# Kernel tuning notes

Measured on AMD Instinct MI355X. Metric: run time of the kernel, lower is better.

## Reference

```python
import jax, jax.numpy as jnp
import numpy as np

N = 50000      # nodes
D_IN = 128     # input_dim
D_OUT = 128    # output_dim
K = 4          # number of core adjacencies (len(adj_list))
E = 600000     # edges per adjacency
LN_EPS = 1e-5


def setup_inputs() -> dict:
    key = jax.random.key(0)
    ks = jax.random.split(key, 9)
    x = jax.random.normal(ks[0], (N, D_IN), dtype=jnp.float32)
    rows = jax.random.randint(ks[1], (K, E), 0, N, dtype=jnp.int32)
    cols = jax.random.randint(ks[2], (K, E), 0, N, dtype=jnp.int32)
    vals = jax.random.uniform(ks[3], (K, E), dtype=jnp.float32)
    std = 1.0 / np.sqrt(D_OUT)  # GRUCell.reset_parameters uniform(-std, std)
    w_x = jax.random.uniform(ks[4], (3 * D_OUT, D_IN), jnp.float32, -std, std)
    b_x = jax.random.uniform(ks[5], (3 * D_OUT,), jnp.float32, -std, std)
    w_h = jax.random.uniform(ks[6], (3 * D_OUT, D_OUT), jnp.float32, -std, std)
    b_h = jax.random.uniform(ks[7], (3 * D_OUT,), jnp.float32, -std, std)
    ln_g = jnp.ones((D_OUT,), jnp.float32)
    ln_b = jnp.zeros((D_OUT,), jnp.float32)
    return {"x": x, "vals": vals, "w_x": w_x, "b_x": b_x, "w_h": w_h,
            "b_h": b_h, "ln_g": ln_g, "ln_b": ln_b, "rows": rows, "cols": cols}


def reference(x, vals, w_x, b_x, w_h, b_h, ln_g, ln_b, rows, cols):
    n = x.shape[0]

    def step(h, inp):
        r, c, v = inp  # COO sparse adj for this diffusion step
        # torch.sparse.mm(adj, x): gather source rows, scale, scatter-add to dest
        msg = v[:, None] * x[c]                              # [E, D_IN]
        res = jax.nn.relu(jax.ops.segment_sum(msg, r, num_segments=n))
        # GRUCell
        gate_x = res @ w_x.T + b_x                           # [N, 3*D_OUT]
        gate_h = h @ w_h.T + b_h
        i_r, i_i, i_n = jnp.split(gate_x, 3, axis=1)
        h_r, h_i, h_n = jnp.split(gate_h, 3, axis=1)
        resetgate = jax.nn.sigmoid(i_r + h_r)
        inputgate = jax.nn.sigmoid(i_i + h_i)
        newgate = jnp.tanh(i_n + resetgate * h_n)
        hy = newgate + inputgate * (h - newgate)
        return hy, None

    # adj_list = adj_list[::-1]
    h0 = jnp.zeros((n, D_OUT), dtype=x.dtype)
    h, _ = jax.lax.scan(step, h0, (rows[::-1], cols[::-1], vals[::-1]))
    # LayerNorm(output_dim)
    mean = jnp.mean(h, axis=-1, keepdims=True)
    var = jnp.var(h, axis=-1, keepdims=True)
    return (h - mean) / jnp.sqrt(var + LN_EPS) * ln_g + ln_b
```

## Files before the change

kernel.cpp:

```cpp
#include <hip/hip_runtime.h>
#include <cstdint>

#define NN 50000
#define DD 128
#define EE 600000
#define NBK 49
#define BCAP 14336

typedef __attribute__((ext_vector_type(8))) short bf16x8;
typedef __attribute__((ext_vector_type(4))) float f32x4;

__device__ __forceinline__ float sigmoid_f(float x) {
    return 1.0f / (1.0f + __expf(-x));
}
__device__ __forceinline__ float tanh_f(float x) {
    float e = __expf(-2.0f * fabsf(x));
    float t = (1.0f - e) / (1.0f + e);
    return copysignf(t, x);
}
__device__ __forceinline__ unsigned short bf16_rn(float v) {
    unsigned u = __float_as_uint(v);
    u = u + 0x7fffu + ((u >> 16) & 1u);
    return (unsigned short)(u >> 16);
}
__device__ __forceinline__ float bf16_tf(unsigned short h) {
    return __uint_as_float(((unsigned)h) << 16);
}

__global__ __launch_bounds__(256) void pack_w_kernel(const float* __restrict__ wx,
                                                     const float* __restrict__ wh,
                                                     unsigned short* __restrict__ Wp) {
    int idx = blockIdx.x * 256 + threadIdx.x;
    if (idx >= 24 * 512 * 32) return;
    int k8 = idx & 31;
    int n = (idx >> 5) & 511;
    int kb = idx >> 14;
    int grp = kb >> 2;
    int k = (kb & 3) * 32 + k8;
    float v = 0.f;
    if (grp < 3) {
        if (n < 384) v = wx[n * 128 + k];
    } else {
        if (n < 256) v = wh[n * 128 + k];
        else if (n >= 384) v = wh[(n - 128) * 128 + k];
    }
    unsigned short hi = bf16_rn(v);
    bool lo = (grp == 2) || (grp == 5);
    Wp[idx] = lo ? bf16_rn(v - bf16_tf(hi)) : hi;
}


__global__ __launch_bounds__(256) void bhist_kernel(const int* __restrict__ rows,
                                                    int* __restrict__ bcnt4) {
    __shared__ int lc[NBK];
    const int tid = threadIdx.x;
    const int k = blockIdx.y;
    const int e0 = blockIdx.x * 2048;
    if (tid < NBK) lc[tid] = 0;
    __syncthreads();
    #pragma unroll
    for (int i = 0; i < 8; ++i) {
        int e = e0 + i * 256 + tid;
        if (e < EE) atomicAdd(&lc[rows[(size_t)k * EE + e] >> 10], 1);
    }
    __syncthreads();
    if (tid < NBK && lc[tid]) atomicAdd(&bcnt4[k * NBK + tid], lc[tid]);
}

__global__ __launch_bounds__(64) void bscan_kernel(const int* __restrict__ bcnt4,
                                                   int* __restrict__ bbase4,
                                                   int* __restrict__ bcur4) {
    int k = threadIdx.x;
    if (k < 4) {
        int run = 0;
        for (int b = 0; b < NBK; ++b) {
            bbase4[k * NBK + b] = run;
            bcur4[k * NBK + b] = run;
            run += bcnt4[k * NBK + b];
        }
    }
}

__global__ __launch_bounds__(256) void bscat_kernel(const int* __restrict__ rows,
                                                    const int* __restrict__ cols,
                                                    const float* __restrict__ vals,
                                                    int* __restrict__ bcur4,
                                                    int2* __restrict__ st2) {
    __shared__ int lcnt[4][NBK];
    __shared__ int sstart4[4][NBK];
    __shared__ int sstart_b[NBK];
    __shared__ int gbase[NBK];
    __shared__ int ltot;
    __shared__ int sw0[2048];
    __shared__ int sw1[2048];
    __shared__ unsigned char sbk[2048];

    const int tid = threadIdx.x;
    const int w = tid >> 6;
    const int k = blockIdx.y;
    const int e0 = blockIdx.x * 2048;

    if (tid < NBK) { lcnt[0][tid] = 0; lcnt[1][tid] = 0; lcnt[2][tid] = 0; lcnt[3][tid] = 0; }
    __syncthreads();

    int eb[8], er[8], ew0[8], ew1[8];
    #pragma unroll
    for (int i = 0; i < 8; ++i) {
        int e = e0 + i * 256 + tid;
        eb[i] = -1;
        if (e < EE) {
            size_t off = (size_t)k * EE + e;
            int r = rows[off];
            int b = r >> 10;
            eb[i] = b;
            er[i] = atomicAdd(&lcnt[w][b], 1);
            ew0[i] = ((r & 1023) << 17) | cols[off];
            ew1[i] = __float_as_int(vals[off]);
        }
    }
    __syncthreads();
    if (tid == 0) {
        int run = 0;
        for (int b = 0; b < NBK; ++b) {
            sstart_b[b] = run;
            #pragma unroll
            for (int q = 0; q < 4; ++q) { sstart4[q][b] = run; run += lcnt[q][b]; }
        }
        ltot = run;
    }
    __syncthreads();
    if (tid < NBK) {
        int n = (sstart4[3][tid] + lcnt[3][tid]) - sstart_b[tid];
        if (n) gbase[tid] = atomicAdd(&bcur4[k * NBK + tid], n);
    }
    __syncthreads();
    #pragma unroll
    for (int i = 0; i < 8; ++i) {
        if (eb[i] >= 0) {
            int slot = sstart4[w][eb[i]] + er[i];
            sw0[slot] = ew0[i];
            sw1[slot] = ew1[i];
            sbk[slot] = (unsigned char)eb[i];
        }
    }
    __syncthreads();
    const int tot = ltot;
    #pragma unroll
    for (int i = 0; i < 8; ++i) {
        int slot = i * 256 + tid;
        if (slot < tot) {
            int b = sbk[slot];
            int pos = gbase[b] + (slot - sstart_b[b]);
            st2[(size_t)k * EE + pos] = make_int2(sw0[slot], sw1[slot]);
        }
    }
}

__global__ __launch_bounds__(1024, 1) void sort2_kernel(const int2* __restrict__ st2,
                                                        const int* __restrict__ bbase4,
                                                        const int* __restrict__ bcnt4,
                                                        int* __restrict__ row_ptr4,
                                                        int2* __restrict__ epair4) {
    __shared__ int cnt[1024];
    __shared__ int cur[1024];
    __shared__ int2 obuf[BCAP];

    const int tid = threadIdx.x;
    const int b = blockIdx.x;
    const int k = blockIdx.y;
    const int base = bbase4[k * NBK + b];
    const int n = bcnt4[k * NBK + b];

    cnt[tid] = 0;
    __syncthreads();
    for (int i = tid; i < n; i += 1024)
        atomicAdd(&cnt[st2[(size_t)k * EE + base + i].x >> 17], 1);
    __syncthreads();

    int v = cnt[tid];
    cur[tid] = v;
    __syncthreads();
    for (int d = 1; d < 1024; d <<= 1) {
        int t = (tid >= d) ? cur[tid - d] : 0;
        __syncthreads();
        cur[tid] += t;
        __syncthreads();
    }
    int excl = cur[tid] - v;

    int grow = b * 1024 + tid;
    if (grow <= NN) row_ptr4[k * (NN + 1) + grow] = base + excl;

    cur[tid] = excl;
    __syncthreads();
    for (int i = tid; i < n; i += 1024) {
        int2 p = st2[(size_t)k * EE + base + i];
        int rl = p.x >> 17;
        int pos = atomicAdd(&cur[rl], 1);
        if (pos < BCAP) obuf[pos] = make_int2(p.x & 0x1FFFF, p.y);
    }
    __syncthreads();
    for (int i = tid; i < n; i += 1024)
        epair4[(size_t)k * EE + base + i] = obuf[i];
}

template <bool FIRST, bool LAST>
__global__ __launch_bounds__(512, 4)
void gemm_gru_kernel(const float* __restrict__ x,
                     const int* __restrict__ row_ptr,
                     const int2* __restrict__ epair,
                     unsigned int* __restrict__ Hpk,
                     float* __restrict__ hout,
                     const unsigned short* __restrict__ Wp,
                     const float* __restrict__ bx,
                     const float* __restrict__ bh) {
    __shared__ unsigned short sA[2 * 64 * 128];

    const int tid = threadIdx.x;
    const int row0 = blockIdx.x * 64;
    const int lane = tid & 63;
    const int w = tid >> 6;
    const int g = lane >> 4;
    const int m16 = lane & 15;

    {
        const int hw = tid >> 5;
        const int l32 = tid & 31;
        const int d0 = l32 * 4;
        #pragma unroll
        for (int p = 0; p < 4; ++p) {
            int rl = p * 16 + hw;
            int grow = row0 + rl;
            float4 a0 = make_float4(0.f, 0.f, 0.f, 0.f);
            float4 a1 = a0, a2 = a0, a3 = a0;
            if (grow < NN) {
                int start = row_ptr[grow];
                int end = row_ptr[grow + 1];
                int e = start;
                for (; e + 3 < end; e += 4) {
                    int2 p0 = epair[e], p1 = epair[e + 1], p2 = epair[e + 2], p3 = epair[e + 3];
                    float4 x0 = *reinterpret_cast<const float4*>(x + (size_t)p0.x * DD + d0);
                    float4 x1 = *reinterpret_cast<const float4*>(x + (size_t)p1.x * DD + d0);
                    float4 x2 = *reinterpret_cast<const float4*>(x + (size_t)p2.x * DD + d0);
                    float4 x3 = *reinterpret_cast<const float4*>(x + (size_t)p3.x * DD + d0);
                    float v0 = __int_as_float(p0.y), v1 = __int_as_float(p1.y);
                    float v2 = __int_as_float(p2.y), v3 = __int_as_float(p3.y);
                    a0.x += v0 * x0.x; a0.y += v0 * x0.y; a0.z += v0 * x0.z; a0.w += v0 * x0.w;
                    a1.x += v1 * x1.x; a1.y += v1 * x1.y; a1.z += v1 * x1.z; a1.w += v1 * x1.w;
                    a2.x += v2 * x2.x; a2.y += v2 * x2.y; a2.z += v2 * x2.z; a2.w += v2 * x2.w;
                    a3.x += v3 * x3.x; a3.y += v3 * x3.y; a3.z += v3 * x3.z; a3.w += v3 * x3.w;
                }
                for (; e < end; ++e) {
                    int2 p0 = epair[e];
                    float v0 = __int_as_float(p0.y);
                    float4 x0 = *reinterpret_cast<const float4*>(x + (size_t)p0.x * DD + d0);
                    a0.x += v0 * x0.x; a0.y += v0 * x0.y; a0.z += v0 * x0.z; a0.w += v0 * x0.w;
                }
            }
            float o[4];
            o[0] = fmaxf((a0.x + a1.x) + (a2.x + a3.x), 0.f);
            o[1] = fmaxf((a0.y + a1.y) + (a2.y + a3.y), 0.f);
            o[2] = fmaxf((a0.z + a1.z) + (a2.z + a3.z), 0.f);
            o[3] = fmaxf((a0.w + a1.w) + (a2.w + a3.w), 0.f);
            ushort4 vh, vl;
            unsigned short h0 = bf16_rn(o[0]); vh.x = h0; vl.x = bf16_rn(o[0] - bf16_tf(h0));
            unsigned short h1 = bf16_rn(o[1]); vh.y = h1; vl.y = bf16_rn(o[1] - bf16_tf(h1));
            unsigned short h2 = bf16_rn(o[2]); vh.z = h2; vl.z = bf16_rn(o[2] - bf16_tf(h2));
            unsigned short h3 = bf16_rn(o[3]); vh.w = h3; vl.w = bf16_rn(o[3] - bf16_tf(h3));
            int slot = l32 >> 1;
            int sw = slot ^ (rl & 7);
            int bi = ((0 * 64 + rl) * 16 + sw) * 8 + (d0 & 7);
            *reinterpret_cast<ushort4*>(sA + bi) = vh;
            *reinterpret_cast<ushort4*>(sA + (64 * 128) + bi) = vl;
        }
    }
    __syncthreads();

    f32x4 acc[4][4];
    #pragma unroll
    for (int G = 0; G < 4; ++G)
        #pragma unroll
        for (int mt = 0; mt < 4; ++mt)
            acc[G][mt] = (f32x4){0.f, 0.f, 0.f, 0.f};

    auto stageH = [&]() {
        #pragma unroll
        for (int it = 0; it < 4; ++it) {
            int idx = it * 512 + tid;
            int row = idx >> 5;
            int j0 = (idx & 31) * 4;
            int grow = row0 + row;
            uint4 v = make_uint4(0, 0, 0, 0);
            if (grow < NN)
                v = *reinterpret_cast<const uint4*>(Hpk + (size_t)grow * 128 + j0);
            ushort4 hh = make_ushort4(v.x & 0xFFFF, v.y & 0xFFFF, v.z & 0xFFFF, v.w & 0xFFFF);
            ushort4 hl = make_ushort4(v.x >> 16, v.y >> 16, v.z >> 16, v.w >> 16);
            int sw = (j0 >> 3) ^ (row & 7);
            int b0 = ((0 * 64 + row) * 16 + sw) * 8 + (j0 & 7);
            int b1 = ((1 * 64 + row) * 16 + sw) * 8 + (j0 & 7);
            *reinterpret_cast<ushort4*>(sA + b0) = hh;
            *reinterpret_cast<ushort4*>(sA + b1) = hl;
        }
    };

    auto do_kb2 = [&](int kbW, int kq, int arr, int G0, int G1, int G2) {
        bf16x8 bfr[3];
        const int Gs[3] = {G0, G1, G2};
        #pragma unroll
        for (int i = 0; i < 3; ++i) {
            int n = Gs[i] * 128 + w * 16 + m16;
            bfr[i] = *reinterpret_cast<const bf16x8*>(
                Wp + ((size_t)(kbW * 512 + n)) * 32 + g * 8);
        }
        bf16x8 afr[4];
        #pragma unroll
        for (int mt = 0; mt < 4; ++mt) {
            int row = mt * 16 + m16;
            int sw = (kq * 4 + g) ^ (row & 7);
            afr[mt] = *reinterpret_cast<const bf16x8*>(
                sA + ((arr * 64 + row) * 16 + sw) * 8);
        }
        __builtin_amdgcn_s_setprio(1);
        #pragma unroll
        for (int mt = 0; mt < 4; ++mt) {
            acc[G0][mt] = __builtin_amdgcn_mfma_f32_16x16x32_bf16(afr[mt], bfr[0], acc[G0][mt], 0, 0, 0);
            acc[G1][mt] = __builtin_amdgcn_mfma_f32_16x16x32_bf16(afr[mt], bfr[1], acc[G1][mt], 0, 0, 0);
            acc[G2][mt] = __builtin_amdgcn_mfma_f32_16x16x32_bf16(afr[mt], bfr[2], acc[G2][mt], 0, 0, 0);
        }
        __builtin_amdgcn_s_setprio(0);
    };

    for (int kq = 0; kq < 4; ++kq) {
        do_kb2(kq,     kq, 0, 0, 1, 2);
        do_kb2(kq,     kq, 1, 0, 1, 2);
        do_kb2(8 + kq, kq, 0, 0, 1, 2);
    }

    if (!FIRST) {
        __syncthreads();
        stageH();
        __syncthreads();
        for (int kq = 0; kq < 4; ++kq) {
            do_kb2(12 + kq, kq, 0, 0, 1, 3);
            do_kb2(12 + kq, kq, 1, 0, 1, 3);
            do_kb2(20 + kq, kq, 0, 0, 1, 3);
        }
    }

    {
        int j = w * 16 + m16;
        float bxr = bx[j], bxi = bx[128 + j], bxn = bx[256 + j];
        float bhr = bh[j], bhi = bh[128 + j], bhn = bh[256 + j];
        #pragma unroll
        for (int mt = 0; mt < 4; ++mt) {
            #pragma unroll
            for (int ii = 0; ii < 4; ++ii) {
                int lrow = mt * 16 + g * 4 + ii;
                int grow = row0 + lrow;
                if (grow >= NN) continue;
                float rr = acc[0][mt][ii] + bxr + bhr;
                float ri = acc[1][mt][ii] + bxi + bhi;
                float rin = acc[2][mt][ii] + bxn;
                float rhn = bhn;
                float ho = 0.f;
                if (!FIRST) {
                    rhn += acc[3][mt][ii];
                    int sw = (j >> 3) ^ (lrow & 7);
                    int bi = (lrow * 16 + sw) * 8 + (j & 7);
                    ho = bf16_tf(sA[bi]) + bf16_tf(sA[64 * 128 + bi]);
                }
                float rg = sigmoid_f(rr);
                float ig = sigmoid_f(ri);
                float ng = tanh_f(rin + rg * rhn);
                float hy = ng + ig * (ho - ng);
                if (LAST) {
                    hout[(size_t)grow * 128 + j] = hy;
                } else {
                    unsigned short hh = bf16_rn(hy);
                    unsigned short hl = bf16_rn(hy - bf16_tf(hh));
                    Hpk[(size_t)grow * 128 + j] = (unsigned)hh | ((unsigned)hl << 16);
                }
            }
        }
    }
}

__global__ __launch_bounds__(256) void ln_kernel(float* __restrict__ h,
                                                 const float* __restrict__ g,
                                                 const float* __restrict__ b) {
    int tid = threadIdx.x;
    int lane = tid & 31;
    int rl = tid >> 5;
    int row = blockIdx.x * 8 + rl;
    if (row >= NN) return;
    float4 v = *reinterpret_cast<const float4*>(h + (size_t)row * DD + lane * 4);
    float s = v.x + v.y + v.z + v.w;
    #pragma unroll
    for (int m = 16; m >= 1; m >>= 1) s += __shfl_xor(s, m, 64);
    float mean = s * (1.0f / DD);
    float dx = v.x - mean, dy = v.y - mean, dz = v.z - mean, dw = v.w - mean;
    float q = dx * dx + dy * dy + dz * dz + dw * dw;
    #pragma unroll
    for (int m = 16; m >= 1; m >>= 1) q += __shfl_xor(q, m, 64);
    float var = q * (1.0f / DD);
    float inv = 1.0f / sqrtf(var + 1e-5f);
    float4 gv = *reinterpret_cast<const float4*>(g + lane * 4);
    float4 bv = *reinterpret_cast<const float4*>(b + lane * 4);
    float4 o;
    o.x = dx * inv * gv.x + bv.x;
    o.y = dy * inv * gv.y + bv.y;
    o.z = dz * inv * gv.z + bv.z;
    o.w = dw * inv * gv.w + bv.w;
    *reinterpret_cast<float4*>(h + (size_t)row * DD + lane * 4) = o;
}

static inline size_t align_up(size_t v, size_t a) { return (v + a - 1) & ~(a - 1); }

extern "C" void kernel_launch(void* const* d_in, const int* in_sizes, int n_in,
                              void* d_out, int out_size, void* d_ws, size_t ws_size,
                              hipStream_t stream) {
    const float* x    = (const float*)d_in[0];
    const float* vals = (const float*)d_in[1];
    const float* wx   = (const float*)d_in[2];
    const float* bx   = (const float*)d_in[3];
    const float* wh   = (const float*)d_in[4];
    const float* bh   = (const float*)d_in[5];
    const float* lng  = (const float*)d_in[6];
    const float* lnb  = (const float*)d_in[7];
    const int* rows   = (const int*)d_in[8];
    const int* cols   = (const int*)d_in[9];

    float* hout = (float*)d_out;

    size_t off = 0;
    char* wsb = (char*)d_ws;
    int2* st2 = (int2*)(wsb + off);     off = align_up(off + (size_t)4 * EE * 8, 256);
    unsigned int* Hpk = (unsigned int*)(wsb + off);    off = align_up(off + (size_t)NN * DD * 4, 256);
    unsigned short* Wp = (unsigned short*)(wsb + off); off = align_up(off + (size_t)24 * 512 * 32 * 2, 256);
    int* row_ptr4 = (int*)(wsb + off);  off = align_up(off + (size_t)4 * (NN + 1) * 4, 256);
    int2* epair4 = (int2*)(wsb + off);  off = align_up(off + (size_t)4 * EE * 8, 256);
    int* bcnt4 = (int*)(wsb + off);     off = align_up(off + (size_t)4 * NBK * 4, 256);
    int* bbase4 = (int*)(wsb + off);    off = align_up(off + (size_t)4 * NBK * 4, 256);
    int* bcur4 = (int*)(wsb + off);     off = align_up(off + (size_t)4 * NBK * 4, 256);

    (void)in_sizes; (void)n_in; (void)out_size; (void)ws_size;

    pack_w_kernel<<<1536, 256, 0, stream>>>(wx, wh, Wp);

    hipMemsetAsync(bcnt4, 0, (size_t)4 * NBK * sizeof(int), stream);
    dim3 e2grid((EE + 2047) / 2048, 4);
    bhist_kernel<<<e2grid, 256, 0, stream>>>(rows, bcnt4);
    bscan_kernel<<<1, 64, 0, stream>>>(bcnt4, bbase4, bcur4);
    bscat_kernel<<<e2grid, 256, 0, stream>>>(rows, cols, vals, bcur4, st2);
    dim3 sgrid(NBK, 4);
    sort2_kernel<<<sgrid, 1024, 0, stream>>>(st2, bbase4, bcnt4, row_ptr4, epair4);

    const int mgrid = (NN + 63) / 64;

    for (int s = 0; s < 4; ++s) {
        int k = 3 - s;
        const int* rp = row_ptr4 + (size_t)k * (NN + 1);
        const int2* ep = epair4 + (size_t)k * EE;
        if (s == 0)
            gemm_gru_kernel<true, false><<<mgrid, 512, 0, stream>>>(
                x, rp, ep, Hpk, hout, Wp, bx, bh);
        else if (s < 3)
            gemm_gru_kernel<false, false><<<mgrid, 512, 0, stream>>>(
                x, rp, ep, Hpk, hout, Wp, bx, bh);
        else
            gemm_gru_kernel<false, true><<<mgrid, 512, 0, stream>>>(
                x, rp, ep, Hpk, hout, Wp, bx, bh);
    }

    ln_kernel<<<(NN + 7) / 8, 256, 0, stream>>>(hout, lng, lnb);
}
```

Before: 401.7 us.

## Fuse four GRU diffusion steps into one kernel keeping hidden state in LDS

Replaces the four per-step gemm_gru launches with a single kernel that loops over the four adjacencies. Each block keeps its 64-row hidden state in shared memory, which is valid because the GRU update is row-local and the aggregation only reads x. This removes the global write and read of the packed hidden state and three kernel launches. The extra 32 KB of LDS per block may cut occupancy below the launch-bounds target.

```diff
diff --git a/kernel.cpp b/kernel.cpp
--- a/kernel.cpp
+++ b/kernel.cpp
@@ -204,17 +204,16 @@
         epair4[(size_t)k * EE + base + i] = obuf[i];
 }
 
-template <bool FIRST, bool LAST>
 __global__ __launch_bounds__(512, 4)
-void gemm_gru_kernel(const float* __restrict__ x,
-                     const int* __restrict__ row_ptr,
-                     const int2* __restrict__ epair,
-                     unsigned int* __restrict__ Hpk,
-                     float* __restrict__ hout,
-                     const unsigned short* __restrict__ Wp,
-                     const float* __restrict__ bx,
-                     const float* __restrict__ bh) {
+void mega_kernel(const float* __restrict__ x,
+                 const int* __restrict__ row_ptr4,
+                 const int2* __restrict__ epair4,
+                 float* __restrict__ hout,
+                 const unsigned short* __restrict__ Wp,
+                 const float* __restrict__ bx,
+                 const float* __restrict__ bh) {
     __shared__ unsigned short sA[2 * 64 * 128];
+    __shared__ unsigned int hLds[64 * 128];
 
     const int tid = threadIdx.x;
     const int row0 = blockIdx.x * 64;
@@ -223,76 +222,13 @@
     const int g = lane >> 4;
     const int m16 = lane & 15;
 
-    {
-        const int hw = tid >> 5;
-        const int l32 = tid & 31;
-        const int d0 = l32 * 4;
-        #pragma unroll
-        for (int p = 0; p < 4; ++p) {
-            int rl = p * 16 + hw;
-            int grow = row0 + rl;
-            float4 a0 = make_float4(0.f, 0.f, 0.f, 0.f);
-            float4 a1 = a0, a2 = a0, a3 = a0;
-            if (grow < NN) {
-                int start = row_ptr[grow];
-                int end = row_ptr[grow + 1];
-                int e = start;
-                for (; e + 3 < end; e += 4) {
-                    int2 p0 = epair[e], p1 = epair[e + 1], p2 = epair[e + 2], p3 = epair[e + 3];
-                    float4 x0 = *reinterpret_cast<const float4*>(x + (size_t)p0.x * DD + d0);
-                    float4 x1 = *reinterpret_cast<const float4*>(x + (size_t)p1.x * DD + d0);
-                    float4 x2 = *reinterpret_cast<const float4*>(x + (size_t)p2.x * DD + d0);
-                    float4 x3 = *reinterpret_cast<const float4*>(x + (size_t)p3.x * DD + d0);
-                    float v0 = __int_as_float(p0.y), v1 = __int_as_float(p1.y);
-                    float v2 = __int_as_float(p2.y), v3 = __int_as_float(p3.y);
-                    a0.x += v0 * x0.x; a0.y += v0 * x0.y; a0.z += v0 * x0.z; a0.w += v0 * x0.w;
-                    a1.x += v1 * x1.x; a1.y += v1 * x1.y; a1.z += v1 * x1.z; a1.w += v1 * x1.w;
-                    a2.x += v2 * x2.x; a2.y += v2 * x2.y; a2.z += v2 * x2.z; a2.w += v2 * x2.w;
-                    a3.x += v3 * x3.x; a3.y += v3 * x3.y; a3.z += v3 * x3.z; a3.w += v3 * x3.w;
-                }
-                for (; e < end; ++e) {
-                    int2 p0 = epair[e];
-                    float v0 = __int_as_float(p0.y);
-                    float4 x0 = *reinterpret_cast<const float4*>(x + (size_t)p0.x * DD + d0);
-                    a0.x += v0 * x0.x; a0.y += v0 * x0.y; a0.z += v0 * x0.z; a0.w += v0 * x0.w;
-                }
-            }
-            float o[4];
-            o[0] = fmaxf((a0.x + a1.x) + (a2.x + a3.x), 0.f);
-            o[1] = fmaxf((a0.y + a1.y) + (a2.y + a3.y), 0.f);
-            o[2] = fmaxf((a0.z + a1.z) + (a2.z + a3.z), 0.f);
-            o[3] = fmaxf((a0.w + a1.w) + (a2.w + a3.w), 0.f);
-            ushort4 vh, vl;
-            unsigned short h0 = bf16_rn(o[0]); vh.x = h0; vl.x = bf16_rn(o[0] - bf16_tf(h0));
-            unsigned short h1 = bf16_rn(o[1]); vh.y = h1; vl.y = bf16_rn(o[1] - bf16_tf(h1));
-            unsigned short h2 = bf16_rn(o[2]); vh.z = h2; vl.z = bf16_rn(o[2] - bf16_tf(h2));
-            unsigned short h3 = bf16_rn(o[3]); vh.w = h3; vl.w = bf16_rn(o[3] - bf16_tf(h3));
-            int slot = l32 >> 1;
-            int sw = slot ^ (rl & 7);
-            int bi = ((0 * 64 + rl) * 16 + sw) * 8 + (d0 & 7);
-            *reinterpret_cast<ushort4*>(sA + bi) = vh;
-            *reinterpret_cast<ushort4*>(sA + (64 * 128) + bi) = vl;
-        }
-    }
-    __syncthreads();
-
-    f32x4 acc[4][4];
-    #pragma unroll
-    for (int G = 0; G < 4; ++G)
-        #pragma unroll
-        for (int mt = 0; mt < 4; ++mt)
-            acc[G][mt] = (f32x4){0.f, 0.f, 0.f, 0.f};
-
     auto stageH = [&]() {
         #pragma unroll
         for (int it = 0; it < 4; ++it) {
             int idx = it * 512 + tid;
             int row = idx >> 5;
             int j0 = (idx & 31) * 4;
-            int grow = row0 + row;
-            uint4 v = make_uint4(0, 0, 0, 0);
-            if (grow < NN)
-                v = *reinterpret_cast<const uint4*>(Hpk + (size_t)grow * 128 + j0);
+            uint4 v = *reinterpret_cast<const uint4*>(&hLds[row * 128 + j0]);
             ushort4 hh = make_ushort4(v.x & 0xFFFF, v.y & 0xFFFF, v.z & 0xFFFF, v.w & 0xFFFF);
             ushort4 hl = make_ushort4(v.x >> 16, v.y >> 16, v.z >> 16, v.w >> 16);
             int sw = (j0 >> 3) ^ (row & 7);
@@ -302,6 +238,8 @@
             *reinterpret_cast<ushort4*>(sA + b1) = hl;
         }
     };
+
+    f32x4 acc[4][4];
 
     auto do_kb2 = [&](int kbW, int kq, int arr, int G0, int G1, int G2) {
         bf16x8 bfr[3];
@@ -330,55 +268,125 @@
         __builtin_amdgcn_s_setprio(0);
     };
 
-    for (int kq = 0; kq < 4; ++kq) {
-        do_kb2(kq,     kq, 0, 0, 1, 2);
-        do_kb2(kq,     kq, 1, 0, 1, 2);
-        do_kb2(8 + kq, kq, 0, 0, 1, 2);
-    }
-
-    if (!FIRST) {
+    #pragma unroll
+    for (int s = 0; s < 4; ++s) {
+        const bool first = (s == 0);
+        const bool last = (s == 3);
+        const int kadj = 3 - s;
+        const int* __restrict__ rp = row_ptr4 + kadj * (NN + 1);
+        const int2* __restrict__ ep = epair4 + (size_t)kadj * EE;
+
+        if (s > 0) __syncthreads();
+
+        {
+            const int hw = tid >> 5;
+            const int l32 = tid & 31;
+            const int d0 = l32 * 4;
+            #pragma unroll
+            for (int p = 0; p < 4; ++p) {
+                int rl = p * 16 + hw;
+                int grow = row0 + rl;
+                float4 a0 = make_float4(0.f, 0.f, 0.f, 0.f);
+                float4 a1 = a0, a2 = a0, a3 = a0;
+                if (grow < NN) {
+                    int start = rp[grow];
+                    int end = rp[grow + 1];
+                    int e = start;
+                    for (; e + 3 < end; e += 4) {
+                        int2 p0 = ep[e], p1 = ep[e + 1], p2 = ep[e + 2], p3 = ep[e + 3];
+                        float4 x0 = *reinterpret_cast<const float4*>(x + (size_t)p0.x * DD + d0);
+                        float4 x1 = *reinterpret_cast<const float4*>(x + (size_t)p1.x * DD + d0);
+                        float4 x2 = *reinterpret_cast<const float4*>(x + (size_t)p2.x * DD + d0);
+                        float4 x3 = *reinterpret_cast<const float4*>(x + (size_t)p3.x * DD + d0);
+                        float v0 = __int_as_float(p0.y), v1 = __int_as_float(p1.y);
+                        float v2 = __int_as_float(p2.y), v3 = __int_as_float(p3.y);
+                        a0.x += v0 * x0.x; a0.y += v0 * x0.y; a0.z += v0 * x0.z; a0.w += v0 * x0.w;
+                        a1.x += v1 * x1.x; a1.y += v1 * x1.y; a1.z += v1 * x1.z; a1.w += v1 * x1.w;
+                        a2.x += v2 * x2.x; a2.y += v2 * x2.y; a2.z += v2 * x2.z; a2.w += v2 * x2.w;
+                        a3.x += v3 * x3.x; a3.y += v3 * x3.y; a3.z += v3 * x3.z; a3.w += v3 * x3.w;
+                    }
+                    for (; e < end; ++e) {
+                        int2 p0 = ep[e];
+                        float v0 = __int_as_float(p0.y);
+                        float4 x0 = *reinterpret_cast<const float4*>(x + (size_t)p0.x * DD + d0);
+                        a0.x += v0 * x0.x; a0.y += v0 * x0.y; a0.z += v0 * x0.z; a0.w += v0 * x0.w;
+                    }
+                }
+                float o[4];
+                o[0] = fmaxf((a0.x + a1.x) + (a2.x + a3.x), 0.f);
+                o[1] = fmaxf((a0.y + a1.y) + (a2.y + a3.y), 0.f);
+                o[2] = fmaxf((a0.z + a1.z) + (a2.z + a3.z), 0.f);
+                o[3] = fmaxf((a0.w + a1.w) + (a2.w + a3.w), 0.f);
+                ushort4 vh, vl;
+                unsigned short h0 = bf16_rn(o[0]); vh.x = h0; vl.x = bf16_rn(o[0] - bf16_tf(h0));
+                unsigned short h1 = bf16_rn(o[1]); vh.y = h1; vl.y = bf16_rn(o[1] - bf16_tf(h1));
+                unsigned short h2 = bf16_rn(o[2]); vh.z = h2; vl.z = bf16_rn(o[2] - bf16_tf(h2));
+                unsigned short h3 = bf16_rn(o[3]); vh.w = h3; vl.w = bf16_rn(o[3] - bf16_tf(h3));
+                int slot = l32 >> 1;
+                int sw = slot ^ (rl & 7);
+                int bi = ((0 * 64 + rl) * 16 + sw) * 8 + (d0 & 7);
+                *reinterpret_cast<ushort4*>(sA + bi) = vh;
+                *reinterpret_cast<ushort4*>(sA + (64 * 128) + bi) = vl;
+            }
+        }
         __syncthreads();
-        stageH();
-        __syncthreads();
+
+        #pragma unroll
+        for (int G = 0; G < 4; ++G)
+            #pragma unroll
+            for (int mt = 0; mt < 4; ++mt)
+                acc[G][mt] = (f32x4){0.f, 0.f, 0.f, 0.f};
+
         for (int kq = 0; kq < 4; ++kq) {
-            do_kb2(12 + kq, kq, 0, 0, 1, 3);
-            do_kb2(12 + kq, kq, 1, 0, 1, 3);
-            do_kb2(20 + kq, kq, 0, 0, 1, 3);
-        }
-    }
-
-    {
-        int j = w * 16 + m16;
-        float bxr = bx[j], bxi = bx[128 + j], bxn = bx[256 + j];
-        float bhr = bh[j], bhi = bh[128 + j], bhn = bh[256 + j];
-        #pragma unroll
-        for (int mt = 0; mt < 4; ++mt) {
+            do_kb2(kq,     kq, 0, 0, 1, 2);
+            do_kb2(kq,     kq, 1, 0, 1, 2);
+            do_kb2(8 + kq, kq, 0, 0, 1, 2);
+        }
+
+        if (!first) {
+            __syncthreads();
+            stageH();
+            __syncthreads();
+            for (int kq = 0; kq < 4; ++kq) {
+                do_kb2(12 + kq, kq, 0, 0, 1, 3);
+                do_kb2(12 + kq, kq, 1, 0, 1, 3);
+                do_kb2(20 + kq, kq, 0, 0, 1, 3);
+            }
+        }
+
+        {
+            int j = w * 16 + m16;
+            float bxr = bx[j], bxi = bx[128 + j], bxn = bx[256 + j];
+            float bhr = bh[j], bhi = bh[128 + j], bhn = bh[256 + j];
             #pragma unroll
-            for (int ii = 0; ii < 4; ++ii) {
-                int lrow = mt * 16 + g * 4 + ii;
-                int grow = row0 + lrow;
-                if (grow >= NN) continue;
-                float rr = acc[0][mt][ii] + bxr + bhr;
-                float ri = acc[1][mt][ii] + bxi + bhi;
-                float rin = acc[2][mt][ii] + bxn;
-                float rhn = bhn;
-                float ho = 0.f;
-                if (!FIRST) {
-                    rhn += acc[3][mt][ii];
-                    int sw = (j >> 3) ^ (lrow & 7);
-                    int bi = (lrow * 16 + sw) * 8 + (j & 7);
-                    ho = bf16_tf(sA[bi]) + bf16_tf(sA[64 * 128 + bi]);
-                }
-                float rg = sigmoid_f(rr);
-                float ig = sigmoid_f(ri);
-                float ng = tanh_f(rin + rg * rhn);
-                float hy = ng + ig * (ho - ng);
-                if (LAST) {
-                    hout[(size_t)grow * 128 + j] = hy;
-                } else {
-                    unsigned short hh = bf16_rn(hy);
-                    unsigned short hl = bf16_rn(hy - bf16_tf(hh));
-                    Hpk[(size_t)grow * 128 + j] = (unsigned)hh | ((unsigned)hl << 16);
+            for (int mt = 0; mt < 4; ++mt) {
+                #pragma unroll
+                for (int ii = 0; ii < 4; ++ii) {
+                    int lrow = mt * 16 + g * 4 + ii;
+                    int grow = row0 + lrow;
+                    if (grow >= NN) continue;
+                    float rr = acc[0][mt][ii] + bxr + bhr;
+                    float ri = acc[1][mt][ii] + bxi + bhi;
+                    float rin = acc[2][mt][ii] + bxn;
+                    float rhn = bhn;
+                    float ho = 0.f;
+                    if (!first) {
+                        rhn += acc[3][mt][ii];
+                        int sw = (j >> 3) ^ (lrow & 7);
+                        int bi = (lrow * 16 + sw) * 8 + (j & 7);
+                        ho = bf16_tf(sA[bi]) + bf16_tf(sA[64 * 128 + bi]);
+                    }
+                    float rg = sigmoid_f(rr);
+                    float ig = sigmoid_f(ri);
+                    float ng = tanh_f(rin + rg * rhn);
+                    float hy = ng + ig * (ho - ng);
+                    if (last) {
+                        hout[(size_t)grow * 128 + j] = hy;
+                    } else {
+                        unsigned short hh = bf16_rn(hy);
+                        unsigned short hl = bf16_rn(hy - bf16_tf(hh));
+                        hLds[lrow * 128 + j] = (unsigned)hh | ((unsigned)hl << 16);
+                    }
                 }
             }
         }
@@ -435,7 +443,6 @@
     size_t off = 0;
     char* wsb = (char*)d_ws;
     int2* st2 = (int2*)(wsb + off);     off = align_up(off + (size_t)4 * EE * 8, 256);
-    unsigned int* Hpk = (unsigned int*)(wsb + off);    off = align_up(off + (size_t)NN * DD * 4, 256);
     unsigned short* Wp = (unsigned short*)(wsb + off); off = align_up(off + (size_t)24 * 512 * 32 * 2, 256);
     int* row_ptr4 = (int*)(wsb + off);  off = align_up(off + (size_t)4 * (NN + 1) * 4, 256);
     int2* epair4 = (int2*)(wsb + off);  off = align_up(off + (size_t)4 * EE * 8, 256);
@@ -456,21 +463,7 @@
     sort2_kernel<<<sgrid, 1024, 0, stream>>>(st2, bbase4, bcnt4, row_ptr4, epair4);
 
     const int mgrid = (NN + 63) / 64;
-
-    for (int s = 0; s < 4; ++s) {
-        int k = 3 - s;
-        const int* rp = row_ptr4 + (size_t)k * (NN + 1);
-        const int2* ep = epair4 + (size_t)k * EE;
-        if (s == 0)
-            gemm_gru_kernel<true, false><<<mgrid, 512, 0, stream>>>(
-                x, rp, ep, Hpk, hout, Wp, bx, bh);
-        else if (s < 3)
-            gemm_gru_kernel<false, false><<<mgrid, 512, 0, stream>>>(
-                x, rp, ep, Hpk, hout, Wp, bx, bh);
-        else
-            gemm_gru_kernel<false, true><<<mgrid, 512, 0, stream>>>(
-                x, rp, ep, Hpk, hout, Wp, bx, bh);
-    }
+    mega_kernel<<<mgrid, 512, 0, stream>>>(x, row_ptr4, epair4, hout, Wp, bx, bh);
 
     ln_kernel<<<(NN + 7) / 8, 256, 0, stream>>>(hout, lng, lnb);
 }
```

Result: slower. 572.2 us (+42.4%).

## Split sparse gather from GRU GEMM and co-schedule next-step gather with current GEMM

Applied to the files above, without the earlier changes.

The per-step kernel is split into two block roles. Gather blocks compute relu(A·x) for the next adjacency and write it to global ping-pong bf16 hi/lo buffers. GEMM/GRU blocks read the previous step's gathered rows into LDS and run the GRU. Because the gather does not depend on h, both roles share one launch with interleaved block indices. This is meant to overlap the latency-bound irregular gather with the MFMA work and to give the gather finer-grained blocks. In exchange it adds an extra launch plus the global write and read traffic of the intermediate buffers, and the sort scratch now aliases one of those buffers.

```diff
diff --git a/kernel.cpp b/kernel.cpp
--- a/kernel.cpp
+++ b/kernel.cpp
@@ -206,76 +206,82 @@
 
 template <bool FIRST, bool LAST>
 __global__ __launch_bounds__(512, 4)
-void gemm_gru_kernel(const float* __restrict__ x,
-                     const int* __restrict__ row_ptr,
-                     const int2* __restrict__ epair,
-                     unsigned int* __restrict__ Hpk,
-                     float* __restrict__ hout,
-                     const unsigned short* __restrict__ Wp,
-                     const float* __restrict__ bx,
-                     const float* __restrict__ bh) {
+void fused_step_kernel(const float* __restrict__ x,
+                       const int* __restrict__ rp_g,
+                       const int2* __restrict__ ep_g,
+                       unsigned short* __restrict__ RhW,
+                       unsigned short* __restrict__ RlW,
+                       const unsigned short* __restrict__ RhR,
+                       const unsigned short* __restrict__ RlR,
+                       unsigned int* __restrict__ Hpk,
+                       float* __restrict__ hout,
+                       const unsigned short* __restrict__ Wp,
+                       const float* __restrict__ bx,
+                       const float* __restrict__ bh,
+                       int gemm_cnt, int gather_cnt) {
     __shared__ unsigned short sA[2 * 64 * 128];
 
+    const int bid = blockIdx.x;
     const int tid = threadIdx.x;
-    const int row0 = blockIdx.x * 64;
+
+    bool is_gemm;
+    int idx;
+    if (gather_cnt == 0) { is_gemm = true;  idx = bid; }
+    else if (gemm_cnt == 0) { is_gemm = false; idx = bid; }
+    else if (bid % 5 == 0) { is_gemm = true;  idx = bid / 5; }
+    else { is_gemm = false; idx = bid - bid / 5 - 1; }
+
+    if (!is_gemm) {
+        const int hw = tid >> 5;
+        const int l32 = tid & 31;
+        const int d0 = l32 * 4;
+        const int row = idx * 16 + hw;
+        if (row >= NN) return;
+        const int start = rp_g[row];
+        const int end = rp_g[row + 1];
+        float4 a0 = make_float4(0.f, 0.f, 0.f, 0.f);
+        float4 a1 = a0, a2 = a0, a3 = a0;
+        int e = start;
+        for (; e + 3 < end; e += 4) {
+            int2 p0 = ep_g[e], p1 = ep_g[e + 1], p2 = ep_g[e + 2], p3 = ep_g[e + 3];
+            float4 x0 = *reinterpret_cast<const float4*>(x + (size_t)p0.x * DD + d0);
+            float4 x1 = *reinterpret_cast<const float4*>(x + (size_t)p1.x * DD + d0);
+            float4 x2 = *reinterpret_cast<const float4*>(x + (size_t)p2.x * DD + d0);
+            float4 x3 = *reinterpret_cast<const float4*>(x + (size_t)p3.x * DD + d0);
+            float v0 = __int_as_float(p0.y), v1 = __int_as_float(p1.y);
+            float v2 = __int_as_float(p2.y), v3 = __int_as_float(p3.y);
+            a0.x += v0 * x0.x; a0.y += v0 * x0.y; a0.z += v0 * x0.z; a0.w += v0 * x0.w;
+            a1.x += v1 * x1.x; a1.y += v1 * x1.y; a1.z += v1 * x1.z; a1.w += v1 * x1.w;
+            a2.x += v2 * x2.x; a2.y += v2 * x2.y; a2.z += v2 * x2.z; a2.w += v2 * x2.w;
+            a3.x += v3 * x3.x; a3.y += v3 * x3.y; a3.z += v3 * x3.z; a3.w += v3 * x3.w;
+        }
+        for (; e < end; ++e) {
+            int2 p0 = ep_g[e];
+            float v0 = __int_as_float(p0.y);
+            float4 x0 = *reinterpret_cast<const float4*>(x + (size_t)p0.x * DD + d0);
+            a0.x += v0 * x0.x; a0.y += v0 * x0.y; a0.z += v0 * x0.z; a0.w += v0 * x0.w;
+        }
+        float o[4];
+        o[0] = fmaxf((a0.x + a1.x) + (a2.x + a3.x), 0.f);
+        o[1] = fmaxf((a0.y + a1.y) + (a2.y + a3.y), 0.f);
+        o[2] = fmaxf((a0.z + a1.z) + (a2.z + a3.z), 0.f);
+        o[3] = fmaxf((a0.w + a1.w) + (a2.w + a3.w), 0.f);
+        ushort4 vh, vl;
+        unsigned short h0 = bf16_rn(o[0]); vh.x = h0; vl.x = bf16_rn(o[0] - bf16_tf(h0));
+        unsigned short h1 = bf16_rn(o[1]); vh.y = h1; vl.y = bf16_rn(o[1] - bf16_tf(h1));
+        unsigned short h2 = bf16_rn(o[2]); vh.z = h2; vl.z = bf16_rn(o[2] - bf16_tf(h2));
+        unsigned short h3 = bf16_rn(o[3]); vh.w = h3; vl.w = bf16_rn(o[3] - bf16_tf(h3));
+        *reinterpret_cast<ushort4*>(RhW + (size_t)row * DD + d0) = vh;
+        *reinterpret_cast<ushort4*>(RlW + (size_t)row * DD + d0) = vl;
+        return;
+    }
+
+    const int row0 = idx * 64;
     const int lane = tid & 63;
     const int w = tid >> 6;
     const int g = lane >> 4;
     const int m16 = lane & 15;
 
-    {
-        const int hw = tid >> 5;
-        const int l32 = tid & 31;
-        const int d0 = l32 * 4;
-        #pragma unroll
-        for (int p = 0; p < 4; ++p) {
-            int rl = p * 16 + hw;
-            int grow = row0 + rl;
-            float4 a0 = make_float4(0.f, 0.f, 0.f, 0.f);
-            float4 a1 = a0, a2 = a0, a3 = a0;
-            if (grow < NN) {
-                int start = row_ptr[grow];
-                int end = row_ptr[grow + 1];
-                int e = start;
-                for (; e + 3 < end; e += 4) {
-                    int2 p0 = epair[e], p1 = epair[e + 1], p2 = epair[e + 2], p3 = epair[e + 3];
-                    float4 x0 = *reinterpret_cast<const float4*>(x + (size_t)p0.x * DD + d0);
-                    float4 x1 = *reinterpret_cast<const float4*>(x + (size_t)p1.x * DD + d0);
-                    float4 x2 = *reinterpret_cast<const float4*>(x + (size_t)p2.x * DD + d0);
-                    float4 x3 = *reinterpret_cast<const float4*>(x + (size_t)p3.x * DD + d0);
-                    float v0 = __int_as_float(p0.y), v1 = __int_as_float(p1.y);
-                    float v2 = __int_as_float(p2.y), v3 = __int_as_float(p3.y);
-                    a0.x += v0 * x0.x; a0.y += v0 * x0.y; a0.z += v0 * x0.z; a0.w += v0 * x0.w;
-                    a1.x += v1 * x1.x; a1.y += v1 * x1.y; a1.z += v1 * x1.z; a1.w += v1 * x1.w;
-                    a2.x += v2 * x2.x; a2.y += v2 * x2.y; a2.z += v2 * x2.z; a2.w += v2 * x2.w;
-                    a3.x += v3 * x3.x; a3.y += v3 * x3.y; a3.z += v3 * x3.z; a3.w += v3 * x3.w;
-                }
-                for (; e < end; ++e) {
-                    int2 p0 = epair[e];
-                    float v0 = __int_as_float(p0.y);
-                    float4 x0 = *reinterpret_cast<const float4*>(x + (size_t)p0.x * DD + d0);
-                    a0.x += v0 * x0.x; a0.y += v0 * x0.y; a0.z += v0 * x0.z; a0.w += v0 * x0.w;
-                }
-            }
-            float o[4];
-            o[0] = fmaxf((a0.x + a1.x) + (a2.x + a3.x), 0.f);
-            o[1] = fmaxf((a0.y + a1.y) + (a2.y + a3.y), 0.f);
-            o[2] = fmaxf((a0.z + a1.z) + (a2.z + a3.z), 0.f);
-            o[3] = fmaxf((a0.w + a1.w) + (a2.w + a3.w), 0.f);
-            ushort4 vh, vl;
-            unsigned short h0 = bf16_rn(o[0]); vh.x = h0; vl.x = bf16_rn(o[0] - bf16_tf(h0));
-            unsigned short h1 = bf16_rn(o[1]); vh.y = h1; vl.y = bf16_rn(o[1] - bf16_tf(h1));
-            unsigned short h2 = bf16_rn(o[2]); vh.z = h2; vl.z = bf16_rn(o[2] - bf16_tf(h2));
-            unsigned short h3 = bf16_rn(o[3]); vh.w = h3; vl.w = bf16_rn(o[3] - bf16_tf(h3));
-            int slot = l32 >> 1;
-            int sw = slot ^ (rl & 7);
-            int bi = ((0 * 64 + rl) * 16 + sw) * 8 + (d0 & 7);
-            *reinterpret_cast<ushort4*>(sA + bi) = vh;
-            *reinterpret_cast<ushort4*>(sA + (64 * 128) + bi) = vl;
-        }
-    }
-    __syncthreads();
-
     f32x4 acc[4][4];
     #pragma unroll
     for (int G = 0; G < 4; ++G)
@@ -283,12 +289,31 @@
         for (int mt = 0; mt < 4; ++mt)
             acc[G][mt] = (f32x4){0.f, 0.f, 0.f, 0.f};
 
+    {
+        #pragma unroll
+        for (int it = 0; it < 4; ++it) {
+            int arr = it >> 1;
+            int idx2 = (it & 1) * 512 + tid;
+            int row = idx2 >> 4;
+            int slot = idx2 & 15;
+            int grow = row0 + row;
+            uint4 v = make_uint4(0, 0, 0, 0);
+            if (grow < NN) {
+                const unsigned short* src = arr ? RlR : RhR;
+                v = *reinterpret_cast<const uint4*>(src + (size_t)grow * 128 + slot * 8);
+            }
+            int sw = slot ^ (row & 7);
+            *reinterpret_cast<uint4*>(sA + ((arr * 64 + row) * 16 + sw) * 8) = v;
+        }
+    }
+    __syncthreads();
+
     auto stageH = [&]() {
         #pragma unroll
         for (int it = 0; it < 4; ++it) {
-            int idx = it * 512 + tid;
-            int row = idx >> 5;
-            int j0 = (idx & 31) * 4;
+            int idx2 = it * 512 + tid;
+            int row = idx2 >> 5;
+            int j0 = (idx2 & 31) * 4;
             int grow = row0 + row;
             uint4 v = make_uint4(0, 0, 0, 0);
             if (grow < NN)
@@ -434,7 +459,10 @@
 
     size_t off = 0;
     char* wsb = (char*)d_ws;
-    int2* st2 = (int2*)(wsb + off);     off = align_up(off + (size_t)4 * EE * 8, 256);
+    unsigned short* Rh0 = (unsigned short*)(wsb + off); off = align_up(off + (size_t)NN * DD * 2, 256);
+    unsigned short* Rl0 = (unsigned short*)(wsb + off); off = align_up(off + (size_t)NN * DD * 2, 256);
+    unsigned short* Rh1 = (unsigned short*)(wsb + off); off = align_up(off + (size_t)NN * DD * 2, 256);
+    unsigned short* Rl1 = (unsigned short*)(wsb + off); off = align_up(off + (size_t)NN * DD * 2, 256);
     unsigned int* Hpk = (unsigned int*)(wsb + off);    off = align_up(off + (size_t)NN * DD * 4, 256);
     unsigned short* Wp = (unsigned short*)(wsb + off); off = align_up(off + (size_t)24 * 512 * 32 * 2, 256);
     int* row_ptr4 = (int*)(wsb + off);  off = align_up(off + (size_t)4 * (NN + 1) * 4, 256);
@@ -442,6 +470,7 @@
     int* bcnt4 = (int*)(wsb + off);     off = align_up(off + (size_t)4 * NBK * 4, 256);
     int* bbase4 = (int*)(wsb + off);    off = align_up(off + (size_t)4 * NBK * 4, 256);
     int* bcur4 = (int*)(wsb + off);     off = align_up(off + (size_t)4 * NBK * 4, 256);
+    int2* st2 = (int2*)Rh1;
 
     (void)in_sizes; (void)n_in; (void)out_size; (void)ws_size;
 
@@ -455,22 +484,31 @@
     dim3 sgrid(NBK, 4);
     sort2_kernel<<<sgrid, 1024, 0, stream>>>(st2, bbase4, bcnt4, row_ptr4, epair4);
 
-    const int mgrid = (NN + 63) / 64;
-
-    for (int s = 0; s < 4; ++s) {
-        int k = 3 - s;
-        const int* rp = row_ptr4 + (size_t)k * (NN + 1);
-        const int2* ep = epair4 + (size_t)k * EE;
-        if (s == 0)
-            gemm_gru_kernel<true, false><<<mgrid, 512, 0, stream>>>(
-                x, rp, ep, Hpk, hout, Wp, bx, bh);
-        else if (s < 3)
-            gemm_gru_kernel<false, false><<<mgrid, 512, 0, stream>>>(
-                x, rp, ep, Hpk, hout, Wp, bx, bh);
-        else
-            gemm_gru_kernel<false, true><<<mgrid, 512, 0, stream>>>(
-                x, rp, ep, Hpk, hout, Wp, bx, bh);
-    }
+    const int GEMM_N = (NN + 63) / 64;
+    const int GATH_N = NN / 16;
+    const int MIX_N = GEMM_N * 5;
+    const int COMB_N = 3907;
+
+    const int* rp3 = row_ptr4 + 3 * (NN + 1);
+    const int* rp2 = row_ptr4 + 2 * (NN + 1);
+    const int* rp1 = row_ptr4 + 1 * (NN + 1);
+    const int* rp0 = row_ptr4 + 0 * (NN + 1);
+    const int2* ep3 = epair4 + (size_t)3 * EE;
+    const int2* ep2 = epair4 + (size_t)2 * EE;
+    const int2* ep1 = epair4 + (size_t)1 * EE;
+    const int2* ep0 = epair4 + (size_t)0 * EE;
+    (void)MIX_N;
+
+    fused_step_kernel<true, false><<<GATH_N, 512, 0, stream>>>(
+        x, rp3, ep3, Rh0, Rl0, Rh0, Rl0, Hpk, hout, Wp, bx, bh, 0, GATH_N);
+    fused_step_kernel<true, false><<<COMB_N, 512, 0, stream>>>(
+        x, rp2, ep2, Rh1, Rl1, Rh0, Rl0, Hpk, hout, Wp, bx, bh, GEMM_N, GATH_N);
+    fused_step_kernel<false, false><<<COMB_N, 512, 0, stream>>>(
+        x, rp1, ep1, Rh0, Rl0, Rh1, Rl1, Hpk, hout, Wp, bx, bh, GEMM_N, GATH_N);
+    fused_step_kernel<false, false><<<COMB_N, 512, 0, stream>>>(
+        x, rp0, ep0, Rh1, Rl1, Rh0, Rl0, Hpk, hout, Wp, bx, bh, GEMM_N, GATH_N);
+    fused_step_kernel<false, true><<<GEMM_N, 512, 0, stream>>>(
+        x, rp0, ep0, Rh0, Rl0, Rh1, Rl1, Hpk, hout, Wp, bx, bh, GEMM_N, 0);
 
     ln_kernel<<<(NN + 7) / 8, 256, 0, stream>>>(hout, lng, lnb);
 }
```

Result: no change. 406.2 us (+1.1%).
